# Performance work log

Measured on AMD Instinct MI355X. Metric: run time of the kernel, lower is better.

## Reference

```python
import jax, jax.numpy as jnp
import numpy as np

DIM = 384
NUM_HEADS = 12
HEAD_DIM = DIM // NUM_HEADS
SCALE = HEAD_DIM ** -0.5


def setup_inputs() -> dict:
    key = jax.random.key(0)
    k_x, k_w, k_o = jax.random.split(key, 3)
    B, n, N, C = 2, 64, 256, DIM
    x = jax.random.normal(k_x, (B, n, N, C), dtype=jnp.float32)
    # kaiming_uniform_(a=sqrt(5)) on a (3C, C) matrix -> bound = 1/sqrt(C)
    bound = 1.0 / np.sqrt(C)
    in_proj_weight = jax.random.uniform(k_w, (3 * C, C), dtype=jnp.float32, minval=-bound, maxval=bound)
    in_proj_bias = jnp.zeros((3 * C,), dtype=jnp.float32)
    ob = 1.0 / np.sqrt(C)
    out_proj_weight = jax.random.uniform(k_o, (C, C), dtype=jnp.float32, minval=-ob, maxval=ob)
    return {"x": x, "in_proj_weight": in_proj_weight, "in_proj_bias": in_proj_bias,
            "out_proj_weight": out_proj_weight}


def reference(x, in_proj_weight, in_proj_bias, out_proj_weight):
    B, n, N, C = x.shape
    H, d = NUM_HEADS, C // NUM_HEADS
    # fused QKV projection: F.linear(x, W, b) = x @ W.T + b
    qkv = jnp.einsum('bwnc,oc->bwno', x, in_proj_weight) + in_proj_bias
    q, k, v = jnp.split(qkv, 3, axis=-1)                      # each [B, n, N, C]
    # [B, n, N, C] -> [B, n, H, N, d]
    def heads(t):
        return t.reshape(B, n, N, H, d).transpose(0, 1, 3, 2, 4)
    q = heads(q) * SCALE
    k = heads(k)
    v = heads(v)
    attn = jax.nn.softmax(jnp.einsum('bwhqd,bwhkd->bwhqk', q, k), axis=-1)
    out = jnp.einsum('bwhqk,bwhkd->bwhqd', attn, v)           # [B, n, H, N, d]
    out = out.transpose(0, 1, 3, 2, 4).reshape(B, n, N, C)
    out = jnp.einsum('bwnc,oc->bwno', out, out_proj_weight)   # out_proj has no bias
    return out
```

## Files before the change

kernel.cpp:

```cpp
#include <hip/hip_runtime.h>
#include <hip/hip_bf16.h>

typedef __attribute__((ext_vector_type(4)))  float  f32x4;
typedef __attribute__((ext_vector_type(16))) float  f32x16;
typedef __attribute__((ext_vector_type(8)))  short  bf16x8;
typedef __attribute__((ext_vector_type(8)))  ushort u16x8;

#define C_DIM   384
#define QKV_DIM 1152
#define NHEAD   12
#define HDIM    32
#define NTOK    256

__device__ __forceinline__ ushort f2bf(float f) {
    union { __hip_bfloat16 h; ushort u; } cv;
    cv.h = __float2bfloat16(f);
    return cv.u;
}

__global__ void cvt_kernel(const float* __restrict__ in, ushort* __restrict__ out, int n8) {
    const int stride = gridDim.x * blockDim.x;
    for (int i = blockIdx.x * blockDim.x + threadIdx.x; i < n8; i += stride) {
        const float4 v0 = reinterpret_cast<const float4*>(in)[2 * i];
        const float4 v1 = reinterpret_cast<const float4*>(in)[2 * i + 1];
        union { ushort u[8]; u16x8 v; } o;
        o.u[0] = f2bf(v0.x); o.u[1] = f2bf(v0.y);
        o.u[2] = f2bf(v0.z); o.u[3] = f2bf(v0.w);
        o.u[4] = f2bf(v1.x); o.u[5] = f2bf(v1.y);
        o.u[6] = f2bf(v1.z); o.u[7] = f2bf(v1.w);
        reinterpret_cast<u16x8*>(out)[i] = o.v;
    }
}

template<int BIAS, int OUTF32, int AHB, int OHB>
__global__ __launch_bounds__(256, 2) void gemm_bt_w(const ushort* __restrict__ A,
                                                    const ushort* __restrict__ Bw,
                                                    const float* __restrict__ bias,
                                                    void* __restrict__ Cout,
                                                    int M, int N, int K) {
    __shared__ __align__(16) ushort As[2][128 * 64];
    __shared__ __align__(16) ushort Bs[2][128 * 64];

    const int t    = threadIdx.x;
    const int lane = t & 63;
    const int wave = t >> 6;
    const int wr   = (wave >> 1) * 64;
    const int wc   = (wave & 1) * 64;
    const int lr   = lane & 15;
    const int lg   = lane >> 4;

    const int gx  = gridDim.x;
    const int nwg = gx * gridDim.y;
    const int hw  = blockIdx.y * gx + blockIdx.x;
    const int cpx = nwg >> 3;
    const int lin = (hw & 7) * cpx + (hw >> 3);
    const int by  = lin / gx;
    const int bx  = lin - by * gx;
    const int mBase = by * 128;
    const int nBase = bx * 128;

    f32x4 acc[4][4] = {};
    const int nK = K >> 6;

    auto stage = [&](int kt, int c) {
        const int k0 = kt << 6;
#pragma unroll
        for (int it = 0; it < 4; ++it) {
            const int idx = it * 256 + t;
            const int r   = idx >> 3;
            const int cb  = (idx & 7) ^ (r & 7);
            const ushort* ga;
            if (AHB) {
                const int k = k0 + cb * 8;
                ga = A + ((size_t)(k >> 5) * M + (mBase + r)) * 32 + (k & 31);
            } else {
                ga = A + (size_t)(mBase + r) * K + k0 + cb * 8;
            }
            __builtin_amdgcn_global_load_lds(
                (const __attribute__((address_space(1))) void*)ga,
                (__attribute__((address_space(3))) void*)(&As[c][it * 2048 + wave * 512]),
                16, 0, 0);
        }
#pragma unroll
        for (int it = 0; it < 4; ++it) {
            const int idx = it * 256 + t;
            const int r   = idx >> 3;
            const int cb  = (idx & 7) ^ (r & 7);
            const ushort* gb = Bw + (size_t)(nBase + r) * K + k0 + cb * 8;
            __builtin_amdgcn_global_load_lds(
                (const __attribute__((address_space(1))) void*)gb,
                (__attribute__((address_space(3))) void*)(&Bs[c][it * 2048 + wave * 512]),
                16, 0, 0);
        }
    };

    stage(0, 0);
    int cur = 0;

    for (int kt = 0; kt < nK; ++kt) {
        if (kt + 1 < nK) {
            stage(kt + 1, cur ^ 1);
            asm volatile("s_waitcnt vmcnt(8)" ::: "memory");
        } else {
            asm volatile("s_waitcnt vmcnt(0)" ::: "memory");
        }
        __builtin_amdgcn_s_barrier();
        __builtin_amdgcn_sched_barrier(0);

#pragma unroll
        for (int kk = 0; kk < 2; ++kk) {
            bf16x8 af[4], bfr[4];
#pragma unroll
            for (int m = 0; m < 4; ++m) {
                const int r = wr + m * 16 + lr;
                af[m] = *reinterpret_cast<const bf16x8*>(
                    &As[cur][r * 64 + (((kk * 4 + lg) ^ (r & 7)) << 3)]);
            }
#pragma unroll
            for (int n = 0; n < 4; ++n) {
                const int r = wc + n * 16 + lr;
                bfr[n] = *reinterpret_cast<const bf16x8*>(
                    &Bs[cur][r * 64 + (((kk * 4 + lg) ^ (r & 7)) << 3)]);
            }
#pragma unroll
            for (int m = 0; m < 4; ++m)
#pragma unroll
                for (int n = 0; n < 4; ++n)
                    acc[m][n] = __builtin_amdgcn_mfma_f32_16x16x32_bf16(af[m], bfr[n], acc[m][n], 0, 0, 0);
        }

        __builtin_amdgcn_sched_barrier(0);
        __builtin_amdgcn_s_barrier();
        cur ^= 1;
    }

#pragma unroll
    for (int n = 0; n < 4; ++n) {
        const int col = nBase + wc + n * 16 + lr;
        const float bv = BIAS ? bias[col] : 0.f;
        const int sel  = OHB ? (col / 384) : 0;
        const int c384 = OHB ? (col - sel * 384) : 0;
#pragma unroll
        for (int m = 0; m < 4; ++m) {
            const int row0 = mBase + wr + m * 16 + lg * 4;
#pragma unroll
            for (int j = 0; j < 4; ++j) {
                const float v = acc[m][n][j] + bv;
                const int row = row0 + j;
                if (OUTF32) {
                    reinterpret_cast<float*>(Cout)[(size_t)row * N + col] = v;
                } else if (OHB) {
                    reinterpret_cast<ushort*>(Cout)[
                        ((size_t)(sel * NHEAD + (c384 >> 5)) * M + row) * 32 + (c384 & 31)] = f2bf(v);
                } else {
                    reinterpret_cast<ushort*>(Cout)[(size_t)row * N + col] = f2bf(v);
                }
            }
        }
    }
}

template<int BIAS, int OUTF32, int AHB, int OHB>
__global__ __launch_bounds__(256, 3) void gemm_bt(const ushort* __restrict__ A,
                                                  const ushort* __restrict__ Bw,
                                                  const float* __restrict__ bias,
                                                  void* __restrict__ Cout,
                                                  int M, int N, int K) {
    __shared__ __align__(16) ushort As[2][128 * 64];
    __shared__ __align__(16) ushort Bs[2][64 * 64];

    const int t    = threadIdx.x;
    const int lane = t & 63;
    const int wave = t >> 6;
    const int wr   = (wave >> 1) * 64;
    const int wc   = (wave & 1) * 32;
    const int lr   = lane & 15;
    const int lg   = lane >> 4;

    const int gx  = gridDim.x;
    const int nwg = gx * gridDim.y;
    const int hw  = blockIdx.y * gx + blockIdx.x;
    const int cpx = nwg >> 3;
    const int lin = (hw & 7) * cpx + (hw >> 3);
    const int by  = lin / gx;
    const int bx  = lin - by * gx;
    const int mBase = by * 128;
    const int nBase = bx * 64;

    f32x4 acc[4][2] = {};
    const int nK = K >> 6;

    auto stage = [&](int kt, int c) {
        const int k0 = kt << 6;
#pragma unroll
        for (int it = 0; it < 4; ++it) {
            const int idx = it * 256 + t;
            const int r   = idx >> 3;
            const int cb  = (idx & 7) ^ (r & 7);
            const ushort* ga;
            if (AHB) {
                const int k = k0 + cb * 8;
                ga = A + ((size_t)(k >> 5) * M + (mBase + r)) * 32 + (k & 31);
            } else {
                ga = A + (size_t)(mBase + r) * K + k0 + cb * 8;
            }
            __builtin_amdgcn_global_load_lds(
                (const __attribute__((address_space(1))) void*)ga,
                (__attribute__((address_space(3))) void*)(&As[c][it * 2048 + wave * 512]),
                16, 0, 0);
        }
#pragma unroll
        for (int it = 0; it < 2; ++it) {
            const int idx = it * 256 + t;
            const int r   = idx >> 3;
            const int cb  = (idx & 7) ^ (r & 7);
            const ushort* gb = Bw + (size_t)(nBase + r) * K + k0 + cb * 8;
            __builtin_amdgcn_global_load_lds(
                (const __attribute__((address_space(1))) void*)gb,
                (__attribute__((address_space(3))) void*)(&Bs[c][it * 2048 + wave * 512]),
                16, 0, 0);
        }
    };

    stage(0, 0);
    int cur = 0;

    for (int kt = 0; kt < nK; ++kt) {
        if (kt + 1 < nK) {
            stage(kt + 1, cur ^ 1);
            asm volatile("s_waitcnt vmcnt(6)" ::: "memory");
        } else {
            asm volatile("s_waitcnt vmcnt(0)" ::: "memory");
        }
        __builtin_amdgcn_s_barrier();
        __builtin_amdgcn_sched_barrier(0);

#pragma unroll
        for (int kk = 0; kk < 2; ++kk) {
            bf16x8 af[4], bfr[2];
#pragma unroll
            for (int m = 0; m < 4; ++m) {
                const int r = wr + m * 16 + lr;
                af[m] = *reinterpret_cast<const bf16x8*>(
                    &As[cur][r * 64 + (((kk * 4 + lg) ^ (r & 7)) << 3)]);
            }
#pragma unroll
            for (int n = 0; n < 2; ++n) {
                const int r = wc + n * 16 + lr;
                bfr[n] = *reinterpret_cast<const bf16x8*>(
                    &Bs[cur][r * 64 + (((kk * 4 + lg) ^ (r & 7)) << 3)]);
            }
#pragma unroll
            for (int m = 0; m < 4; ++m)
#pragma unroll
                for (int n = 0; n < 2; ++n)
                    acc[m][n] = __builtin_amdgcn_mfma_f32_16x16x32_bf16(af[m], bfr[n], acc[m][n], 0, 0, 0);
        }

        __builtin_amdgcn_sched_barrier(0);
        __builtin_amdgcn_s_barrier();
        cur ^= 1;
    }

#pragma unroll
    for (int n = 0; n < 2; ++n) {
        const int col = nBase + wc + n * 16 + lr;
        const float bv = BIAS ? bias[col] : 0.f;
        const int sel  = OHB ? (col / 384) : 0;
        const int c384 = OHB ? (col - sel * 384) : 0;
#pragma unroll
        for (int m = 0; m < 4; ++m) {
            const int row0 = mBase + wr + m * 16 + lg * 4;
#pragma unroll
            for (int j = 0; j < 4; ++j) {
                const float v = acc[m][n][j] + bv;
                const int row = row0 + j;
                if (OUTF32) {
                    reinterpret_cast<float*>(Cout)[(size_t)row * N + col] = v;
                } else if (OHB) {
                    reinterpret_cast<ushort*>(Cout)[
                        ((size_t)(sel * NHEAD + (c384 >> 5)) * M + row) * 32 + (c384 & 31)] = f2bf(v);
                } else {
                    reinterpret_cast<ushort*>(Cout)[(size_t)row * N + col] = f2bf(v);
                }
            }
        }
    }
}

__global__ __launch_bounds__(512) void attn_kernel(const ushort* __restrict__ qkv,
                                                   ushort* __restrict__ att,
                                                   int Mtok) {
    __shared__ __align__(16) ushort Ks[NTOK * HDIM];
    __shared__ __align__(16) ushort Vt[HDIM * NTOK];

    const int bid = blockIdx.x;
    const int win = bid / NHEAD;
    const int h   = bid % NHEAD;

    const int t    = threadIdx.x;
    const int lane = t & 63;
    const int wave = t >> 6;
    const int l31  = lane & 31;
    const int h5   = lane >> 5;

    const size_t winRow = (size_t)win * NTOK;
    const ushort* Qbase = qkv + ((size_t)h * Mtok + winRow) * HDIM;
    const ushort* Kbase = qkv + ((size_t)(NHEAD + h) * Mtok + winRow) * HDIM;
    const ushort* Vbase = qkv + ((size_t)(2 * NHEAD + h) * Mtok + winRow) * HDIM;

#pragma unroll
    for (int it = 0; it < 2; ++it) {
        const int idx = it * 512 + t;
        const int key = idx >> 2;
        const int cb  = (idx & 3) ^ (key & 3);
        const ushort* gk = Kbase + key * HDIM + cb * 8;
        __builtin_amdgcn_global_load_lds(
            (const __attribute__((address_space(1))) void*)gk,
            (__attribute__((address_space(3))) void*)(&Ks[it * 4096 + wave * 512]),
            16, 0, 0);
    }
#pragma unroll
    for (int it = 0; it < 2; ++it) {
        const int idx = it * 512 + t;
        const int key = idx >> 2;
        const int cb  = idx & 3;
        u16x8 v8 = *reinterpret_cast<const u16x8*>(Vbase + key * HDIM + cb * 8);
#pragma unroll
        for (int jj = 0; jj < 8; ++jj) {
            const int dd  = cb * 8 + jj;
            const int blk = (key >> 3) ^ (dd & 7) ^ ((2 * (dd >> 3)) & 6);
            Vt[dd * NTOK + blk * 8 + (key & 7)] = v8[jj];
        }
    }
    __syncthreads();

    const float c1   = 0.25503509f;
    const int   vmsk = (l31 & 7) ^ ((2 * (l31 >> 3)) & 6);
    const int   kmsk = l31 & 3;
    const int   q0   = wave * 32;

    const int qrow = q0 + l31;
    const bf16x8 qf0 = *reinterpret_cast<const bf16x8*>(
        Qbase + (size_t)qrow * HDIM + h5 * 8);
    const bf16x8 qf1 = *reinterpret_cast<const bf16x8*>(
        Qbase + (size_t)qrow * HDIM + 16 + h5 * 8);

    float sm0 = 0.f, sm1 = 0.f, sm2 = 0.f, sm3 = 0.f;
#pragma unroll
    for (int tt = 0; tt < 8; ++tt) {
        const int key = tt * 32 + l31;
        const bf16x8 kf0 = *reinterpret_cast<const bf16x8*>(
            &Ks[key * HDIM + ((h5 ^ kmsk) << 3)]);
        const bf16x8 kf1 = *reinterpret_cast<const bf16x8*>(
            &Ks[key * HDIM + (((2 + h5) ^ kmsk) << 3)]);
        f32x16 s = {};
        s = __builtin_amdgcn_mfma_f32_32x32x16_bf16(kf0, qf0, s, 0, 0, 0);
        s = __builtin_amdgcn_mfma_f32_32x32x16_bf16(kf1, qf1, s, 0, 0, 0);
#pragma unroll
        for (int r = 0; r < 16; r += 4) {
            sm0 += __builtin_amdgcn_exp2f(s[r + 0] * c1);
            sm1 += __builtin_amdgcn_exp2f(s[r + 1] * c1);
            sm2 += __builtin_amdgcn_exp2f(s[r + 2] * c1);
            sm3 += __builtin_amdgcn_exp2f(s[r + 3] * c1);
        }
    }
    float sm = (sm0 + sm1) + (sm2 + sm3);
    sm += __shfl_xor(sm, 32, 64);
    const float inv = __builtin_amdgcn_rcpf(sm);

    f32x16 O = {};
#pragma unroll
    for (int tt = 0; tt < 8; ++tt) {
        const int key = tt * 32 + l31;
        const bf16x8 kf0 = *reinterpret_cast<const bf16x8*>(
            &Ks[key * HDIM + ((h5 ^ kmsk) << 3)]);
        const bf16x8 kf1 = *reinterpret_cast<const bf16x8*>(
            &Ks[key * HDIM + (((2 + h5) ^ kmsk) << 3)]);
        f32x16 s = {};
        s = __builtin_amdgcn_mfma_f32_32x32x16_bf16(kf0, qf0, s, 0, 0, 0);
        s = __builtin_amdgcn_mfma_f32_32x32x16_bf16(kf1, qf1, s, 0, 0, 0);

        uint pk8[8];
#pragma unroll
        for (int m = 0; m < 8; ++m) {
            const int r = 4 * (m >> 1) + 2 * (m & 1);
            const float lo = __builtin_amdgcn_exp2f(s[r + 0] * c1) * inv;
            const float hi = __builtin_amdgcn_exp2f(s[r + 1] * c1) * inv;
            uint d;
            asm("v_cvt_pk_bf16_f32 %0, %1, %2" : "=v"(d) : "v"(lo), "v"(hi));
            pk8[m] = d;
        }

#pragma unroll
        for (int k16 = 0; k16 < 2; ++k16) {
            const int mb = 4 * k16;
            const uint s0 = h5 ? pk8[mb + 0] : pk8[mb + 2];
            const uint s1 = h5 ? pk8[mb + 1] : pk8[mb + 3];
            const uint x0 = (uint)__shfl_xor((int)s0, 32, 64);
            const uint x1 = (uint)__shfl_xor((int)s1, 32, 64);
            union { uint u[4]; bf16x8 v; } pw;
            pw.u[0] = h5 ? x0 : pk8[mb + 0];
            pw.u[1] = h5 ? x1 : pk8[mb + 1];
            pw.u[2] = h5 ? pk8[mb + 2] : x0;
            pw.u[3] = h5 ? pk8[mb + 3] : x1;
            const int blk = (4 * tt + 2 * k16 + h5) ^ vmsk;
            const bf16x8 vf = *reinterpret_cast<const bf16x8*>(
                &Vt[l31 * NTOK + blk * 8]);
            O = __builtin_amdgcn_mfma_f32_32x32x16_bf16(pw.v, vf, O, 0, 0, 0);
        }
    }

    ushort* obase = att + ((size_t)h * Mtok + winRow + q0) * HDIM + l31;
#pragma unroll
    for (int r = 0; r < 16; ++r) {
        const int qr = (r & 3) + 8 * (r >> 2) + 4 * h5;
        obase[(size_t)qr * HDIM] = f2bf(O[r]);
    }
}

extern "C" void kernel_launch(void* const* d_in, const int* in_sizes, int n_in,
                              void* d_out, int out_size, void* d_ws, size_t ws_size,
                              hipStream_t stream) {
    const float* x     = (const float*)d_in[0];
    const float* w_in  = (const float*)d_in[1];
    const float* b_in  = (const float*)d_in[2];
    const float* w_out = (const float*)d_in[3];

    const int M    = in_sizes[0] / C_DIM;
    const int nWin = M / NTOK;

    char* ws = (char*)d_ws;
    size_t off = 0;
    ushort* xb    = (ushort*)(ws + off); off += (size_t)M * C_DIM * 2;
    ushort* qkvb  = (ushort*)(ws + off); off += (size_t)M * QKV_DIM * 2;
    ushort* attb  = (ushort*)(ws + off); off += (size_t)M * C_DIM * 2;
    ushort* wqkvb = (ushort*)(ws + off); off += (size_t)QKV_DIM * C_DIM * 2;
    ushort* woutb = (ushort*)(ws + off);

    cvt_kernel<<<2048, 256, 0, stream>>>(x, xb, M * C_DIM / 8);
    cvt_kernel<<<(QKV_DIM * C_DIM / 8 + 255) / 256, 256, 0, stream>>>(
        w_in, wqkvb, QKV_DIM * C_DIM / 8);
    cvt_kernel<<<(C_DIM * C_DIM / 8 + 255) / 256, 256, 0, stream>>>(
        w_out, woutb, C_DIM * C_DIM / 8);

    gemm_bt_w<1, 0, 0, 1><<<dim3(QKV_DIM / 128, M / 128), 256, 0, stream>>>(
        xb, wqkvb, b_in, qkvb, M, QKV_DIM, C_DIM);

    attn_kernel<<<nWin * NHEAD, 512, 0, stream>>>(qkvb, attb, M);

    gemm_bt<0, 1, 1, 0><<<dim3(C_DIM / 64, M / 128), 256, 0, stream>>>(
        attb, woutb, nullptr, d_out, M, C_DIM, C_DIM);
}
```

Baseline: 117.7 us.

## Fuse fp32-to-bf16 input conversion into QKV GEMM A-tile loading

Drops the separate conversion pass over x and has the QKV GEMM load fp32 activations straight into registers. Each thread converts them to bf16 and writes the swizzled tile into LDS, while B tiles still use direct global-to-LDS loads. This removes one full read and write of the bf16 copy of x plus a kernel launch. In exchange the GEMM reads twice as many bytes for A, uses more registers, and adds conversion ALU work inside the pipelined loop.

```diff
diff --git a/kernel.cpp b/kernel.cpp
--- a/kernel.cpp
+++ b/kernel.cpp
@@ -32,11 +32,11 @@
     }
 }
 
-template<int BIAS, int OUTF32, int AHB, int OHB>
-__global__ __launch_bounds__(256, 2) void gemm_bt_w(const ushort* __restrict__ A,
+template<int BIAS, int OHB>
+__global__ __launch_bounds__(256, 2) void gemm_af32(const float* __restrict__ Af,
                                                     const ushort* __restrict__ Bw,
                                                     const float* __restrict__ bias,
-                                                    void* __restrict__ Cout,
+                                                    ushort* __restrict__ Cout,
                                                     int M, int N, int K) {
     __shared__ __align__(16) ushort As[2][128 * 64];
     __shared__ __align__(16) ushort Bs[2][128 * 64];
@@ -62,25 +62,33 @@
     f32x4 acc[4][4] = {};
     const int nK = K >> 6;
 
-    auto stage = [&](int kt, int c) {
+    float4 a0[4], a1[4];
+    auto ldA = [&](int kt) {
         const int k0 = kt << 6;
 #pragma unroll
         for (int it = 0; it < 4; ++it) {
             const int idx = it * 256 + t;
             const int r   = idx >> 3;
             const int cb  = (idx & 7) ^ (r & 7);
-            const ushort* ga;
-            if (AHB) {
-                const int k = k0 + cb * 8;
-                ga = A + ((size_t)(k >> 5) * M + (mBase + r)) * 32 + (k & 31);
-            } else {
-                ga = A + (size_t)(mBase + r) * K + k0 + cb * 8;
-            }
-            __builtin_amdgcn_global_load_lds(
-                (const __attribute__((address_space(1))) void*)ga,
-                (__attribute__((address_space(3))) void*)(&As[c][it * 2048 + wave * 512]),
-                16, 0, 0);
-        }
+            const float* ga = Af + (size_t)(mBase + r) * K + k0 + cb * 8;
+            a0[it] = *reinterpret_cast<const float4*>(ga);
+            a1[it] = *reinterpret_cast<const float4*>(ga + 4);
+        }
+    };
+    auto wrA = [&](int c) {
+#pragma unroll
+        for (int it = 0; it < 4; ++it) {
+            const int idx = it * 256 + t;
+            union { ushort u[8]; u16x8 v; } pw;
+            pw.u[0] = f2bf(a0[it].x); pw.u[1] = f2bf(a0[it].y);
+            pw.u[2] = f2bf(a0[it].z); pw.u[3] = f2bf(a0[it].w);
+            pw.u[4] = f2bf(a1[it].x); pw.u[5] = f2bf(a1[it].y);
+            pw.u[6] = f2bf(a1[it].z); pw.u[7] = f2bf(a1[it].w);
+            *reinterpret_cast<u16x8*>(&As[c][(size_t)idx * 8]) = pw.v;
+        }
+    };
+    auto issueB = [&](int kt, int c) {
+        const int k0 = kt << 6;
 #pragma unroll
         for (int it = 0; it < 4; ++it) {
             const int idx = it * 256 + t;
@@ -93,20 +101,7 @@
                 16, 0, 0);
         }
     };
-
-    stage(0, 0);
-    int cur = 0;
-
-    for (int kt = 0; kt < nK; ++kt) {
-        if (kt + 1 < nK) {
-            stage(kt + 1, cur ^ 1);
-            asm volatile("s_waitcnt vmcnt(8)" ::: "memory");
-        } else {
-            asm volatile("s_waitcnt vmcnt(0)" ::: "memory");
-        }
-        __builtin_amdgcn_s_barrier();
-        __builtin_amdgcn_sched_barrier(0);
-
+    auto compute = [&](int c) {
 #pragma unroll
         for (int kk = 0; kk < 2; ++kk) {
             bf16x8 af[4], bfr[4];
@@ -114,13 +109,13 @@
             for (int m = 0; m < 4; ++m) {
                 const int r = wr + m * 16 + lr;
                 af[m] = *reinterpret_cast<const bf16x8*>(
-                    &As[cur][r * 64 + (((kk * 4 + lg) ^ (r & 7)) << 3)]);
+                    &As[c][r * 64 + (((kk * 4 + lg) ^ (r & 7)) << 3)]);
             }
 #pragma unroll
             for (int n = 0; n < 4; ++n) {
                 const int r = wc + n * 16 + lr;
                 bfr[n] = *reinterpret_cast<const bf16x8*>(
-                    &Bs[cur][r * 64 + (((kk * 4 + lg) ^ (r & 7)) << 3)]);
+                    &Bs[c][r * 64 + (((kk * 4 + lg) ^ (r & 7)) << 3)]);
             }
 #pragma unroll
             for (int m = 0; m < 4; ++m)
@@ -128,9 +123,27 @@
                 for (int n = 0; n < 4; ++n)
                     acc[m][n] = __builtin_amdgcn_mfma_f32_16x16x32_bf16(af[m], bfr[n], acc[m][n], 0, 0, 0);
         }
-
-        __builtin_amdgcn_sched_barrier(0);
-        __builtin_amdgcn_s_barrier();
+    };
+
+    ldA(0); issueB(0, 0);
+    asm volatile("s_waitcnt vmcnt(4)" ::: "memory");
+    wrA(0);
+    __syncthreads();
+    int cur = 0;
+
+    for (int kt = 0; kt < nK; ++kt) {
+        const bool more = (kt + 1 < nK);
+        if (more) {
+            ldA(kt + 1);
+            issueB(kt + 1, cur ^ 1);
+            __builtin_amdgcn_sched_barrier(0);
+        }
+        compute(cur);
+        if (more) {
+            asm volatile("s_waitcnt vmcnt(4)" ::: "memory");
+            wrA(cur ^ 1);
+            __syncthreads();
+        }
         cur ^= 1;
     }
 
@@ -147,13 +160,10 @@
             for (int j = 0; j < 4; ++j) {
                 const float v = acc[m][n][j] + bv;
                 const int row = row0 + j;
-                if (OUTF32) {
-                    reinterpret_cast<float*>(Cout)[(size_t)row * N + col] = v;
-                } else if (OHB) {
-                    reinterpret_cast<ushort*>(Cout)[
-                        ((size_t)(sel * NHEAD + (c384 >> 5)) * M + row) * 32 + (c384 & 31)] = f2bf(v);
+                if (OHB) {
+                    Cout[((size_t)(sel * NHEAD + (c384 >> 5)) * M + row) * 32 + (c384 & 31)] = f2bf(v);
                 } else {
-                    reinterpret_cast<ushort*>(Cout)[(size_t)row * N + col] = f2bf(v);
+                    Cout[(size_t)row * N + col] = f2bf(v);
                 }
             }
         }
@@ -432,20 +442,18 @@
 
     char* ws = (char*)d_ws;
     size_t off = 0;
-    ushort* xb    = (ushort*)(ws + off); off += (size_t)M * C_DIM * 2;
     ushort* qkvb  = (ushort*)(ws + off); off += (size_t)M * QKV_DIM * 2;
     ushort* attb  = (ushort*)(ws + off); off += (size_t)M * C_DIM * 2;
     ushort* wqkvb = (ushort*)(ws + off); off += (size_t)QKV_DIM * C_DIM * 2;
     ushort* woutb = (ushort*)(ws + off);
 
-    cvt_kernel<<<2048, 256, 0, stream>>>(x, xb, M * C_DIM / 8);
     cvt_kernel<<<(QKV_DIM * C_DIM / 8 + 255) / 256, 256, 0, stream>>>(
         w_in, wqkvb, QKV_DIM * C_DIM / 8);
     cvt_kernel<<<(C_DIM * C_DIM / 8 + 255) / 256, 256, 0, stream>>>(
         w_out, woutb, C_DIM * C_DIM / 8);
 
-    gemm_bt_w<1, 0, 0, 1><<<dim3(QKV_DIM / 128, M / 128), 256, 0, stream>>>(
-        xb, wqkvb, b_in, qkvb, M, QKV_DIM, C_DIM);
+    gemm_af32<1, 1><<<dim3(QKV_DIM / 128, M / 128), 256, 0, stream>>>(
+        x, wqkvb, b_in, qkvb, M, QKV_DIM, C_DIM);
 
     attn_kernel<<<nWin * NHEAD, 512, 0, stream>>>(qkvb, attb, M);
 
```

After: 119.3 us. No clear change (+1.3%).
